# Kernel optimization log

Hardware: AMD Instinct MI355X
Metric: run time of the kernel (lower is better)

## Reference

```python
import jax, jax.numpy as jnp
import numpy as np

N_A, N_C, N_L = 50000, 10000, 10000
HID = 128


def _gatv2(x_src, x_dst, src, dst, ea, Wl, bl, Wr, br, We, att, bias, H):
    # GATv2Conv (PyG) bipartite, edge_dim=1, concat=False (mean over heads), eval mode (no dropout)
    C = bias.shape[0]
    n_dst = x_dst.shape[0]
    xl = (x_src @ Wl + bl).reshape(-1, H, C)      # [N_src, H, C]
    xr = (x_dst @ Wr + br).reshape(-1, H, C)      # [N_dst, H, C]
    e = jax.nn.leaky_relu(xl[src] + xr[dst] + (ea @ We).reshape(-1, H, C), 0.2)  # [E,H,C]
    logit = jnp.einsum('ehc,hc->eh', e, att)      # [E,H]
    m = jax.ops.segment_max(logit, dst, num_segments=n_dst)
    m = jax.lax.stop_gradient(jnp.where(jnp.isfinite(m), m, 0.0))
    ex = jnp.exp(logit - m[dst])
    denom = jax.ops.segment_sum(ex, dst, num_segments=n_dst)
    alpha = ex / (denom[dst] + 1e-16)             # segment softmax over incoming edges
    out = jax.ops.segment_sum(alpha[:, :, None] * xl[src], dst, num_segments=n_dst)
    return out.mean(axis=1) + bias                # concat=False -> head mean + bias


def setup_inputs() -> dict:
    key = jax.random.key(0)
    ks = iter(jax.random.split(key, 80))
    def rn(shape, s=1.0):
        return jax.random.normal(next(ks), shape, jnp.float32) * s
    inp = {}
    inp['x_asset'] = rn((N_A, 512))
    inp['x_creator'] = rn((N_C, 2))
    inp['x_licensee'] = rn((N_L, 1))
    # edges: (name, E, src_max, dst_max)
    edges = [('cb', 50000, N_A, N_C), ('lt', 100000, N_A, N_L), ('sim', 200000, N_A, N_A),
             ('fw', 100000, N_A, N_A), ('rcb', 50000, N_C, N_A), ('rlt', 100000, N_L, N_A)]
    for name, E, smax, dmax in edges:
        inp[f'{name}_src'] = jax.random.randint(next(ks), (E,), 0, smax, jnp.int32)
        inp[f'{name}_dst'] = jax.random.randint(next(ks), (E,), 0, dmax, jnp.int32)
        inp[f'ea_{name}'] = rn((E, 1))
    w = 0.05  # param scale
    inp['Wp_a'] = rn((512, HID), w); inp['bp_a'] = rn((HID,), w)
    inp['Wp_c'] = rn((2, HID), w);   inp['bp_c'] = rn((HID,), w)
    inp['Wp_l'] = rn((1, HID), w);   inp['bp_l'] = rn((HID,), w)
    # layer 1: heads=2, stacked over the 6 relations
    H1 = 2
    inp['Wl1'] = rn((6, HID, H1 * HID), w); inp['bl1'] = rn((6, H1 * HID), w)
    inp['Wr1'] = rn((6, HID, H1 * HID), w); inp['br1'] = rn((6, H1 * HID), w)
    inp['We1'] = rn((6, 1, H1 * HID), w)
    inp['att1'] = rn((6, H1, HID), w); inp['bias1'] = rn((6, HID), w)
    # layer 2: heads=1
    inp['Wl2'] = rn((6, HID, HID), w); inp['bl2'] = rn((6, HID), w)
    inp['Wr2'] = rn((6, HID, HID), w); inp['br2'] = rn((6, HID), w)
    inp['We2'] = rn((6, 1, HID), w)
    inp['att2'] = rn((6, 1, HID), w); inp['bias2'] = rn((6, HID), w)
    inp['Wc1'] = rn((HID, HID), w); inp['bc1'] = rn((HID,), w)
    inp['Wc2'] = rn((HID, 3), w);   inp['bc2'] = rn((3,), w)
    inp['query_asset_index'] = 123
    return inp


def reference(x_asset, x_creator, x_licensee, Wp_a, bp_a, Wp_c, bp_c, Wp_l, bp_l,
              Wl1, bl1, Wr1, br1, We1, att1, bias1,
              Wl2, bl2, Wr2, br2, We2, att2, bias2,
              Wc1, bc1, Wc2, bc2,
              ea_cb, ea_lt, ea_sim, ea_fw, ea_rcb, ea_rlt,
              cb_src, cb_dst, lt_src, lt_dst, sim_src, sim_dst,
              fw_src, fw_dst, rcb_src, rcb_dst, rlt_src, rlt_dst,
              query_asset_index):
    x = {'Asset': x_asset @ Wp_a + bp_a,
         'Creator': x_creator @ Wp_c + bp_c,
         'Licensee': x_licensee @ Wp_l + bp_l}
    rels = [('Asset', 'Creator', cb_src, cb_dst, ea_cb),
            ('Asset', 'Licensee', lt_src, lt_dst, ea_lt),
            ('Asset', 'Asset', sim_src, sim_dst, ea_sim),
            ('Asset', 'Asset', fw_src, fw_dst, ea_fw),
            ('Creator', 'Asset', rcb_src, rcb_dst, ea_rcb),
            ('Licensee', 'Asset', rlt_src, rlt_dst, ea_rlt)]

    def hetero_layer(x, Wl, bl, Wr, br, We, att, bias, H):
        out = {k: jnp.zeros((v.shape[0], HID), v.dtype) for k, v in x.items()}
        for i, (st, dt, s, d, ea) in enumerate(rels):  # HeteroConv aggr='sum'
            out[dt] = out[dt] + _gatv2(x[st], x[dt], s, d, ea,
                                       Wl[i], bl[i], Wr[i], br[i], We[i], att[i], bias[i], H)
        return out

    x = hetero_layer(x, Wl1, bl1, Wr1, br1, We1, att1, bias1, 2)
    x = {k: jax.nn.relu(v) for k, v in x.items()}  # eval: dropout is identity
    x = hetero_layer(x, Wl2, bl2, Wr2, br2, We2, att2, bias2, 1)
    x = {k: jax.nn.relu(v) for k, v in x.items()}
    a = x['Asset'][query_asset_index]
    return jax.nn.relu(a @ Wc1 + bc1) @ Wc2 + bc2
```

## Files before the change

### kernel.cpp

```cpp
#include <hip/hip_runtime.h>
#include <math.h>

#define FAMAX 64
#define FCMAX 32
#define FLMAX 32
#define N1MAX 512
#define N2MAX 128
#define XL2C  24

struct Inputs {
  const float *x_asset, *x_creator, *x_licensee;
  const float *Wp_a,*bp_a,*Wp_c,*bp_c,*Wp_l,*bp_l;
  const float *Wl1,*bl1,*Wr1,*br1,*We1,*att1,*bias1;
  const float *Wl2,*bl2,*Wr2,*br2,*We2,*att2,*bias2;
  const float *Wc1,*bc1,*Wc2,*bc2;
};

struct Edges {
  const int *cb_s,*cb_d;  const float* ea_cb;  int Ecb;
  const int *lt_s,*lt_d;  const float* ea_lt;  int Elt;
  const int *sim_s,*sim_d;const float* ea_sim; int Esim;
  const int *fw_s,*fw_d;  const float* ea_fw;  int Efw;
  const int *rcb_s,*rcb_d;const float* ea_rcb; int Ercb;
  const int *rlt_s,*rlt_d;const float* ea_rlt; int Erlt;
};

struct WSP {
  int* cnt;
  int *fa,*fc,*fl;
  int* l2rel; int* l2src; int* l2slot; float* l2ea;
  int* l1rel; int* l1src; int* l1dslot; float* l1ea;
  float* xl1e;
  float* logit1;
  float *x1a,*x1c,*x1l;
  float* xl2e;
};

__device__ __forceinline__ float leaky(float x){ return x > 0.f ? x : 0.2f*x; }

__device__ __forceinline__ void proj256(int type, int node, const Inputs& in,
                                        float* h0, float* xs, float* part){
  int t = threadIdx.x;
  if (type == 0){
    xs[t]       = in.x_asset[(size_t)node*512 + t];
    xs[t + 256] = in.x_asset[(size_t)node*512 + t + 256];
    __syncthreads();
    int j = t & 127, g2 = t >> 7;
    float acc = 0.f;
    const float* W = in.Wp_a + (size_t)g2*256*128 + j;
    const float* xg = xs + g2*256;
    for (int k=0;k<256;k++) acc = fmaf(xg[k], W[(size_t)k*128], acc);
    part[t] = acc;
    __syncthreads();
    if (t < 128) h0[t] = in.bp_a[t] + part[t] + part[128 + t];
  } else if (type == 1){
    if (t < 128)
      h0[t] = in.bp_c[t] + in.x_creator[node*2]*in.Wp_c[t]
            + in.x_creator[node*2+1]*in.Wp_c[128+t];
  } else {
    if (t < 128)
      h0[t] = in.bp_l[t] + in.x_licensee[node]*in.Wp_l[t];
  }
  __syncthreads();
}

__global__ void k1_scan_l2(Edges eg, const int* qptr, WSP w){
  int q = qptr[0];
  if (blockIdx.x==0 && threadIdx.x==0){
    int s = atomicAdd(&w.cnt[1], 1);
    if (s < FAMAX){ w.fa[s] = q; w.cnt[5] = s; } else w.cnt[5] = 0;
  }
  int total4 = (eg.Esim + eg.Efw + eg.Ercb + eg.Erlt) >> 2;
  for (int i4 = blockIdx.x*blockDim.x + threadIdx.x; i4 < total4; i4 += gridDim.x*blockDim.x){
    int j = i4 << 2, rel; const int *sp,*dp; const float* ep;
    if (j < eg.Esim){ rel=2; sp=eg.sim_s; dp=eg.sim_d; ep=eg.ea_sim; }
    else { j -= eg.Esim;
      if (j < eg.Efw){ rel=3; sp=eg.fw_s; dp=eg.fw_d; ep=eg.ea_fw; }
      else { j -= eg.Efw;
        if (j < eg.Ercb){ rel=4; sp=eg.rcb_s; dp=eg.rcb_d; ep=eg.ea_rcb; }
        else { j -= eg.Ercb; rel=5; sp=eg.rlt_s; dp=eg.rlt_d; ep=eg.ea_rlt; }
      }
    }
    int4 d4 = *(const int4*)(dp + j);
    #pragma unroll
    for (int m=0;m<4;m++){
      int d = (m==0)?d4.x:(m==1)?d4.y:(m==2)?d4.z:d4.w;
      if (d == q){
        int src = sp[j+m];
        int k = atomicAdd(&w.cnt[0], 1);
        if (k < N2MAX){
          w.l2rel[k]=rel; w.l2src[k]=src; w.l2ea[k]=ep[j+m];
          int s, slot = -1;
          if (rel <= 3){ s = atomicAdd(&w.cnt[1],1); if (s<FAMAX){ w.fa[s]=src; slot=s; } }
          else if (rel == 4){ s = atomicAdd(&w.cnt[2],1); if (s<FCMAX){ w.fc[s]=src; slot=s; } }
          else { s = atomicAdd(&w.cnt[3],1); if (s<FLMAX){ w.fl[s]=src; slot=s; } }
          w.l2slot[k] = slot;
        }
      }
    }
  }
}

__global__ void k2_scan_l1(Edges eg, WSP w){
  __shared__ int sfa[FAMAX], sfc[FCMAX], sfl[FLMAX];
  __shared__ int snf[3];
  int t = threadIdx.x;
  if (t < 3){
    int caps[3] = {FAMAX, FCMAX, FLMAX};
    int v = w.cnt[1+t]; snf[t] = v < caps[t] ? v : caps[t];
  }
  if (t < FAMAX) sfa[t] = w.fa[t];
  if (t < FCMAX) sfc[t] = w.fc[t];
  if (t < FLMAX) sfl[t] = w.fl[t];
  __syncthreads();
  int total4 = (eg.Ecb+eg.Elt+eg.Esim+eg.Efw+eg.Ercb+eg.Erlt) >> 2;
  for (int i4 = blockIdx.x*blockDim.x + t; i4 < total4; i4 += gridDim.x*blockDim.x){
    int j = i4 << 2, rel; const int *sp,*dp; const float* ep;
    if (j < eg.Ecb){ rel=0; sp=eg.cb_s; dp=eg.cb_d; ep=eg.ea_cb; }
    else { j -= eg.Ecb;
    if (j < eg.Elt){ rel=1; sp=eg.lt_s; dp=eg.lt_d; ep=eg.ea_lt; }
    else { j -= eg.Elt;
    if (j < eg.Esim){ rel=2; sp=eg.sim_s; dp=eg.sim_d; ep=eg.ea_sim; }
    else { j -= eg.Esim;
    if (j < eg.Efw){ rel=3; sp=eg.fw_s; dp=eg.fw_d; ep=eg.ea_fw; }
    else { j -= eg.Efw;
    if (j < eg.Ercb){ rel=4; sp=eg.rcb_s; dp=eg.rcb_d; ep=eg.ea_rcb; }
    else { j -= eg.Ercb; rel=5; sp=eg.rlt_s; dp=eg.rlt_d; ep=eg.ea_rlt; }}}}}
    const int* lst = (rel==0) ? sfc : (rel==1) ? sfl : sfa;
    int n = (rel==0) ? snf[1] : (rel==1) ? snf[2] : snf[0];
    int4 d4 = *(const int4*)(dp + j);
    #pragma unroll
    for (int m=0;m<4;m++){
      int d = (m==0)?d4.x:(m==1)?d4.y:(m==2)?d4.z:d4.w;
      for (int s=0;s<n;s++){
        if (d == lst[s]){
          int k = atomicAdd(&w.cnt[4], 1);
          if (k < N1MAX){ w.l1rel[k]=rel; w.l1src[k]=sp[j+m]; w.l1dslot[k]=s; w.l1ea[k]=ep[j+m]; }
        }
      }
    }
  }
}

__global__ void k3_edge(Inputs in, WSP w){
  __shared__ float xs[512];
  __shared__ float part[256];
  __shared__ float h0s[128];
  __shared__ float h0d[128];
  __shared__ float red[256];
  int i = blockIdx.x, t = threadIdx.x;
  int n1 = w.cnt[4] < N1MAX ? w.cnt[4] : N1MAX;
  if (i >= n1) return;
  int rel = w.l1rel[i], src = w.l1src[i], dslot = w.l1dslot[i];
  float ea = w.l1ea[i];
  int stype = (rel <= 3) ? 0 : (rel == 4 ? 1 : 2);
  int dtype = (rel == 0) ? 1 : (rel == 1 ? 2 : 0);
  int dnode = (rel == 0) ? w.fc[dslot] : (rel == 1 ? w.fl[dslot] : w.fa[dslot]);
  proj256(stype, src, in, h0s, xs, part);
  float xl1 = in.bl1[rel*256 + t];
  {
    const float* W = in.Wl1 + (size_t)rel*128*256 + t;
    for (int c=0;c<128;c++) xl1 = fmaf(h0s[c], W[(size_t)c*256], xl1);
  }
  w.xl1e[(size_t)i*256 + t] = xl1;
  proj256(dtype, dnode, in, h0d, xs, part);
  float xr1 = in.br1[rel*256 + t];
  {
    const float* W = in.Wr1 + (size_t)rel*128*256 + t;
    for (int c=0;c<128;c++) xr1 = fmaf(h0d[c], W[(size_t)c*256], xr1);
  }
  int h = t >> 7, c = t & 127;
  float e = leaky(xl1 + xr1 + ea*in.We1[rel*256 + t]);
  red[t] = e * in.att1[(rel*2 + h)*128 + c];
  __syncthreads();
  for (int s=64; s>0; s>>=1){ if (c < s) red[t] += red[t+s]; __syncthreads(); }
  if (c == 0) w.logit1[i*2 + h] = red[t];
}

__global__ void k4_agg(Inputs in, WSP w){
  int b = blockIdx.x, j = threadIdx.x;
  int nfa = w.cnt[1] < FAMAX ? w.cnt[1] : FAMAX;
  int nfc = w.cnt[2] < FCMAX ? w.cnt[2] : FCMAX;
  int nfl = w.cnt[3] < FLMAX ? w.cnt[3] : FLMAX;
  int type, slot;
  if (b < FAMAX){ slot=b; if (slot>=nfa) return; type=0; }
  else if (b < FAMAX+FCMAX){ slot=b-FAMAX; if (slot>=nfc) return; type=1; }
  else { slot=b-FAMAX-FCMAX; if (slot>=nfl) return; type=2; }
  int n1 = w.cnt[4] < N1MAX ? w.cnt[4] : N1MAX;
  float out = 0.f;
  int r0, r1;
  if (type==0){ r0=2; r1=5; } else if (type==1){ r0=0; r1=0; } else { r0=1; r1=1; }
  for (int r=r0; r<=r1; r++){
    out += in.bias1[r*128 + j];
    float m0=-INFINITY, m1=-INFINITY;
    for (int i=0;i<n1;i++){
      if (w.l1rel[i]==r && w.l1dslot[i]==slot){
        m0 = fmaxf(m0, w.logit1[i*2]);
        m1 = fmaxf(m1, w.logit1[i*2+1]);
      }
    }
    if (m0 == -INFINITY) continue;
    float d0=0.f, d1=0.f, a0=0.f, a1=0.f;
    for (int i=0;i<n1;i++){
      if (w.l1rel[i]==r && w.l1dslot[i]==slot){
        float e0 = expf(w.logit1[i*2]   - m0);
        float e1 = expf(w.logit1[i*2+1] - m1);
        d0 += e0; d1 += e1;
        a0 = fmaf(e0, w.xl1e[(size_t)i*256 + j],       a0);
        a1 = fmaf(e1, w.xl1e[(size_t)i*256 + 128 + j], a1);
      }
    }
    out += 0.5f*(a0/(d0+1e-16f) + a1/(d1+1e-16f));
  }
  float v = fmaxf(out, 0.f);
  if (type==0) w.x1a[slot*128 + j] = v;
  else if (type==1) w.x1c[slot*128 + j] = v;
  else w.x1l[slot*128 + j] = v;
}

__global__ void k5_final(Inputs in, WSP w, float* outp){
  __shared__ float xq[128];
  __shared__ float xsrc[128];
  __shared__ float xr2s[4][128];
  __shared__ float xl2s[XL2C][128];
  __shared__ float red[128];
  __shared__ float lg2[N2MAX];
  __shared__ int   srl2[N2MAX];
  __shared__ float x2[128];
  __shared__ float tt[128];
  int t = threadIdx.x, j = t & 127, half = t >> 7;
  int n2 = w.cnt[0] < N2MAX ? w.cnt[0] : N2MAX;
  int qs = w.cnt[5]; if (qs >= FAMAX) qs = 0;
  if (t < 128) xq[t] = w.x1a[(size_t)qs*128 + t];
  __syncthreads();
  for (int rr = half; rr < 4; rr += 2){
    int r = 2 + rr;
    float acc = in.br2[r*128 + j];
    const float* W = in.Wr2 + (size_t)r*128*128 + j;
    for (int c=0;c<128;c++) acc = fmaf(xq[c], W[(size_t)c*128], acc);
    xr2s[rr][j] = acc;
  }
  __syncthreads();
  for (int i=0;i<n2;i++){
    int rel = w.l2rel[i], slot = w.l2slot[i];
    if (slot < 0){ if (t==0) srl2[i] = -1; __syncthreads(); continue; }
    const float* xb = (rel<=3) ? w.x1a : (rel==4 ? w.x1c : w.x1l);
    if (t < 128) xsrc[t] = xb[(size_t)slot*128 + t];
    __syncthreads();
    if (t < 128){
      float xl2 = in.bl2[rel*128 + t];
      const float* W = in.Wl2 + (size_t)rel*128*128 + t;
      for (int c=0;c<128;c++) xl2 = fmaf(xsrc[c], W[(size_t)c*128], xl2);
      if (i < XL2C) xl2s[i][t] = xl2;
      else w.xl2e[(size_t)i*128 + t] = xl2;
      float e = leaky(xl2 + xr2s[rel-2][t] + w.l2ea[i]*in.We2[rel*128 + t]);
      red[t] = e * in.att2[rel*128 + t];
    }
    __syncthreads();
    for (int s=64; s>0; s>>=1){ if (t < s) red[t] += red[t+s]; __syncthreads(); }
    if (t == 0){ lg2[i] = red[0]; srl2[i] = rel; }
    __syncthreads();
  }
  if (t < 128){
    float o = 0.f;
    for (int r=2; r<=5; r++){
      o += in.bias2[r*128 + t];
      float m = -INFINITY;
      for (int i=0;i<n2;i++) if (srl2[i]==r) m = fmaxf(m, lg2[i]);
      if (m == -INFINITY) continue;
      float d = 0.f, acc = 0.f;
      for (int i=0;i<n2;i++) if (srl2[i]==r){
        float e = expf(lg2[i] - m);
        d += e;
        float xv = (i < XL2C) ? xl2s[i][t] : w.xl2e[(size_t)i*128 + t];
        acc = fmaf(e, xv, acc);
      }
      o += acc/(d + 1e-16f);
    }
    x2[t] = fmaxf(o, 0.f);
  }
  __syncthreads();
  if (t < 128){
    float acc = in.bc1[t];
    for (int c=0;c<128;c++) acc = fmaf(x2[c], in.Wc1[c*128 + t], acc);
    tt[t] = fmaxf(acc, 0.f);
  }
  __syncthreads();
  if (t < 3){
    float r = in.bc2[t];
    for (int c=0;c<128;c++) r = fmaf(tt[c], in.Wc2[c*3 + t], r);
    outp[t] = r;
  }
}

extern "C" void kernel_launch(void* const* d_in, const int* in_sizes, int n_in,
                              void* d_out, int out_size, void* d_ws, size_t ws_size,
                              hipStream_t stream){
  Inputs in;
  in.x_asset   = (const float*)d_in[0];
  in.x_creator = (const float*)d_in[1];
  in.x_licensee= (const float*)d_in[2];
  Edges eg;
  eg.cb_s =(const int*)d_in[3];  eg.cb_d =(const int*)d_in[4];  eg.ea_cb =(const float*)d_in[5];  eg.Ecb = in_sizes[3];
  eg.lt_s =(const int*)d_in[6];  eg.lt_d =(const int*)d_in[7];  eg.ea_lt =(const float*)d_in[8];  eg.Elt = in_sizes[6];
  eg.sim_s=(const int*)d_in[9];  eg.sim_d=(const int*)d_in[10]; eg.ea_sim=(const float*)d_in[11]; eg.Esim= in_sizes[9];
  eg.fw_s =(const int*)d_in[12]; eg.fw_d =(const int*)d_in[13]; eg.ea_fw =(const float*)d_in[14]; eg.Efw = in_sizes[12];
  eg.rcb_s=(const int*)d_in[15]; eg.rcb_d=(const int*)d_in[16]; eg.ea_rcb=(const float*)d_in[17]; eg.Ercb= in_sizes[15];
  eg.rlt_s=(const int*)d_in[18]; eg.rlt_d=(const int*)d_in[19]; eg.ea_rlt=(const float*)d_in[20]; eg.Erlt= in_sizes[18];
  in.Wp_a=(const float*)d_in[21]; in.bp_a=(const float*)d_in[22];
  in.Wp_c=(const float*)d_in[23]; in.bp_c=(const float*)d_in[24];
  in.Wp_l=(const float*)d_in[25]; in.bp_l=(const float*)d_in[26];
  in.Wl1=(const float*)d_in[27]; in.bl1=(const float*)d_in[28];
  in.Wr1=(const float*)d_in[29]; in.br1=(const float*)d_in[30];
  in.We1=(const float*)d_in[31]; in.att1=(const float*)d_in[32]; in.bias1=(const float*)d_in[33];
  in.Wl2=(const float*)d_in[34]; in.bl2=(const float*)d_in[35];
  in.Wr2=(const float*)d_in[36]; in.br2=(const float*)d_in[37];
  in.We2=(const float*)d_in[38]; in.att2=(const float*)d_in[39]; in.bias2=(const float*)d_in[40];
  in.Wc1=(const float*)d_in[41]; in.bc1=(const float*)d_in[42];
  in.Wc2=(const float*)d_in[43]; in.bc2=(const float*)d_in[44];
  const int* qptr = (const int*)d_in[45];

  char* p = (char*)d_ws;
  auto carve = [&](size_t n)->char*{ char* r = p; p += ((n + 255) & ~(size_t)255); return r; };
  WSP w;
  w.cnt  = (int*)carve(16*4);
  w.fa = (int*)carve(FAMAX*4); w.fc = (int*)carve(FCMAX*4); w.fl = (int*)carve(FLMAX*4);
  w.l2rel=(int*)carve(N2MAX*4); w.l2src=(int*)carve(N2MAX*4); w.l2slot=(int*)carve(N2MAX*4); w.l2ea=(float*)carve(N2MAX*4);
  w.l1rel=(int*)carve(N1MAX*4); w.l1src=(int*)carve(N1MAX*4); w.l1dslot=(int*)carve(N1MAX*4); w.l1ea=(float*)carve(N1MAX*4);
  w.xl1e=(float*)carve((size_t)N1MAX*256*4);
  w.logit1=(float*)carve((size_t)N1MAX*2*4);
  w.x1a=(float*)carve((size_t)FAMAX*128*4);
  w.x1c=(float*)carve((size_t)FCMAX*128*4);
  w.x1l=(float*)carve((size_t)FLMAX*128*4);
  w.xl2e=(float*)carve((size_t)N2MAX*128*4);

  hipMemsetAsync(w.cnt, 0, 16*4, stream);

  int tE2_4 = (eg.Esim + eg.Efw + eg.Ercb + eg.Erlt) >> 2;
  k1_scan_l2<<<(tE2_4+255)/256, 256, 0, stream>>>(eg, qptr, w);
  int tE1_4 = (eg.Ecb + eg.Elt + eg.Esim + eg.Efw + eg.Ercb + eg.Erlt) >> 2;
  k2_scan_l1<<<(tE1_4+255)/256, 256, 0, stream>>>(eg, w);
  k3_edge<<<N1MAX, 256, 0, stream>>>(in, w);
  k4_agg<<<FAMAX + FCMAX + FLMAX, 128, 0, stream>>>(in, w);
  k5_final<<<1, 256, 0, stream>>>(in, w, (float*)d_out);
}
```

Baseline: 327.8 us.

## Split final layer-2 stage into per-edge parallel kernel and small reduction kernel

The single-block final kernel previously looped serially over up to 128 layer-2 edges, doing a 128x128 matvec and a tree reduction for each. This work now runs in a separate kernel with one block per edge, writing projected features and logits to workspace. A small final kernel then does the softmax aggregation and classifier head. The trade-off is an extra launch and recomputing the destination projection in every edge block.

```diff
diff --git a/kernel.cpp b/kernel.cpp
--- a/kernel.cpp
+++ b/kernel.cpp
@@ -6,7 +6,6 @@
 #define FLMAX 32
 #define N1MAX 512
 #define N2MAX 128
-#define XL2C  24
 
 struct Inputs {
   const float *x_asset, *x_creator, *x_licensee;
@@ -34,6 +33,7 @@
   float* logit1;
   float *x1a,*x1c,*x1l;
   float* xl2e;
+  float* logit2;
 };
 
 __device__ __forceinline__ float leaky(float x){ return x > 0.f ? x : 0.2f*x; }
@@ -218,78 +218,72 @@
   else w.x1l[slot*128 + j] = v;
 }
 
-__global__ void k5_final(Inputs in, WSP w, float* outp){
+__global__ void k5b_l2edge(Inputs in, WSP w){
   __shared__ float xq[128];
   __shared__ float xsrc[128];
-  __shared__ float xr2s[4][128];
-  __shared__ float xl2s[XL2C][128];
   __shared__ float red[128];
-  __shared__ float lg2[N2MAX];
-  __shared__ int   srl2[N2MAX];
+  int i = blockIdx.x, j = threadIdx.x;
+  int n2 = w.cnt[0] < N2MAX ? w.cnt[0] : N2MAX;
+  if (i >= n2) return;
+  int rel = w.l2rel[i], slot = w.l2slot[i];
+  float ea = w.l2ea[i];
+  if (slot < 0){
+    w.xl2e[(size_t)i*128 + j] = 0.f;
+    if (j == 0) w.logit2[i] = -INFINITY;
+    return;
+  }
+  const float* xb = (rel<=3) ? w.x1a : (rel==4 ? w.x1c : w.x1l);
+  int qs = w.cnt[5]; if (qs >= FAMAX) qs = 0;
+  xq[j]   = w.x1a[(size_t)qs*128 + j];
+  xsrc[j] = xb[(size_t)slot*128 + j];
+  __syncthreads();
+  float xr2 = in.br2[rel*128 + j];
+  {
+    const float* W = in.Wr2 + (size_t)rel*128*128 + j;
+    for (int c=0;c<128;c++) xr2 = fmaf(xq[c], W[(size_t)c*128], xr2);
+  }
+  float xl2 = in.bl2[rel*128 + j];
+  {
+    const float* W = in.Wl2 + (size_t)rel*128*128 + j;
+    for (int c=0;c<128;c++) xl2 = fmaf(xsrc[c], W[(size_t)c*128], xl2);
+  }
+  w.xl2e[(size_t)i*128 + j] = xl2;
+  float e = leaky(xl2 + xr2 + ea*in.We2[rel*128 + j]);
+  red[j] = e * in.att2[rel*128 + j];
+  __syncthreads();
+  for (int s=64; s>0; s>>=1){ if (j < s) red[j] += red[j+s]; __syncthreads(); }
+  if (j == 0) w.logit2[i] = red[0];
+}
+
+__global__ void k5c_final(Inputs in, WSP w, float* outp){
   __shared__ float x2[128];
   __shared__ float tt[128];
-  int t = threadIdx.x, j = t & 127, half = t >> 7;
+  int j = threadIdx.x;
   int n2 = w.cnt[0] < N2MAX ? w.cnt[0] : N2MAX;
-  int qs = w.cnt[5]; if (qs >= FAMAX) qs = 0;
-  if (t < 128) xq[t] = w.x1a[(size_t)qs*128 + t];
-  __syncthreads();
-  for (int rr = half; rr < 4; rr += 2){
-    int r = 2 + rr;
-    float acc = in.br2[r*128 + j];
-    const float* W = in.Wr2 + (size_t)r*128*128 + j;
-    for (int c=0;c<128;c++) acc = fmaf(xq[c], W[(size_t)c*128], acc);
-    xr2s[rr][j] = acc;
-  }
-  __syncthreads();
-  for (int i=0;i<n2;i++){
-    int rel = w.l2rel[i], slot = w.l2slot[i];
-    if (slot < 0){ if (t==0) srl2[i] = -1; __syncthreads(); continue; }
-    const float* xb = (rel<=3) ? w.x1a : (rel==4 ? w.x1c : w.x1l);
-    if (t < 128) xsrc[t] = xb[(size_t)slot*128 + t];
-    __syncthreads();
-    if (t < 128){
-      float xl2 = in.bl2[rel*128 + t];
-      const float* W = in.Wl2 + (size_t)rel*128*128 + t;
-      for (int c=0;c<128;c++) xl2 = fmaf(xsrc[c], W[(size_t)c*128], xl2);
-      if (i < XL2C) xl2s[i][t] = xl2;
-      else w.xl2e[(size_t)i*128 + t] = xl2;
-      float e = leaky(xl2 + xr2s[rel-2][t] + w.l2ea[i]*in.We2[rel*128 + t]);
-      red[t] = e * in.att2[rel*128 + t];
-    }
-    __syncthreads();
-    for (int s=64; s>0; s>>=1){ if (t < s) red[t] += red[t+s]; __syncthreads(); }
-    if (t == 0){ lg2[i] = red[0]; srl2[i] = rel; }
-    __syncthreads();
-  }
-  if (t < 128){
-    float o = 0.f;
-    for (int r=2; r<=5; r++){
-      o += in.bias2[r*128 + t];
-      float m = -INFINITY;
-      for (int i=0;i<n2;i++) if (srl2[i]==r) m = fmaxf(m, lg2[i]);
-      if (m == -INFINITY) continue;
-      float d = 0.f, acc = 0.f;
-      for (int i=0;i<n2;i++) if (srl2[i]==r){
-        float e = expf(lg2[i] - m);
-        d += e;
-        float xv = (i < XL2C) ? xl2s[i][t] : w.xl2e[(size_t)i*128 + t];
-        acc = fmaf(e, xv, acc);
-      }
-      o += acc/(d + 1e-16f);
-    }
-    x2[t] = fmaxf(o, 0.f);
-  }
-  __syncthreads();
-  if (t < 128){
-    float acc = in.bc1[t];
-    for (int c=0;c<128;c++) acc = fmaf(x2[c], in.Wc1[c*128 + t], acc);
-    tt[t] = fmaxf(acc, 0.f);
-  }
-  __syncthreads();
-  if (t < 3){
-    float r = in.bc2[t];
-    for (int c=0;c<128;c++) r = fmaf(tt[c], in.Wc2[c*3 + t], r);
-    outp[t] = r;
+  float o = 0.f;
+  for (int r=2; r<=5; r++){
+    o += in.bias2[r*128 + j];
+    float m = -INFINITY;
+    for (int i=0;i<n2;i++) if (w.l2rel[i]==r) m = fmaxf(m, w.logit2[i]);
+    if (m == -INFINITY) continue;
+    float d = 0.f, acc = 0.f;
+    for (int i=0;i<n2;i++) if (w.l2rel[i]==r){
+      float e = expf(w.logit2[i] - m);
+      d += e;
+      acc = fmaf(e, w.xl2e[(size_t)i*128 + j], acc);
+    }
+    o += acc/(d + 1e-16f);
+  }
+  x2[j] = fmaxf(o, 0.f);
+  __syncthreads();
+  float acc = in.bc1[j];
+  for (int c=0;c<128;c++) acc = fmaf(x2[c], in.Wc1[c*128 + j], acc);
+  tt[j] = fmaxf(acc, 0.f);
+  __syncthreads();
+  if (j < 3){
+    float r = in.bc2[j];
+    for (int c=0;c<128;c++) r = fmaf(tt[c], in.Wc2[c*3 + j], r);
+    outp[j] = r;
   }
 }
 
@@ -333,6 +327,7 @@
   w.x1c=(float*)carve((size_t)FCMAX*128*4);
   w.x1l=(float*)carve((size_t)FLMAX*128*4);
   w.xl2e=(float*)carve((size_t)N2MAX*128*4);
+  w.logit2=(float*)carve(N2MAX*4);
 
   hipMemsetAsync(w.cnt, 0, 16*4, stream);
 
@@ -342,5 +337,6 @@
   k2_scan_l1<<<(tE1_4+255)/256, 256, 0, stream>>>(eg, w);
   k3_edge<<<N1MAX, 256, 0, stream>>>(in, w);
   k4_agg<<<FAMAX + FCMAX + FLMAX, 128, 0, stream>>>(in, w);
-  k5_final<<<1, 256, 0, stream>>>(in, w, (float*)d_out);
-}
+  k5b_l2edge<<<N2MAX, 128, 0, stream>>>(in, w);
+  k5c_final<<<1, 128, 0, stream>>>(in, w, (float*)d_out);
+}
```

After: 309.2 us. 1.06x faster.
